# Performance work log

Hardware: AMD Instinct MI355X
Metric: run time of the kernel (lower is better)

Reference implementation:

```python
import jax, jax.numpy as jnp
import numpy as np

B, T, D = 1, 2048, 1024
H = 16
HD = D // H
K = 4
FF = 4 * D
LAYERS = 24
EPS = 1.1920929e-07  # torch.finfo(float32).eps, RMSNorm default


def setup_inputs() -> dict:
    key = jax.random.key(0)
    ks = jax.random.split(key, 16)
    s = 0.02
    return {
        "x": jax.random.normal(ks[0], (B, T, D), jnp.float32),
        "gamma": jax.random.uniform(ks[1], (D,), jnp.float32),
        "beta": jax.random.normal(ks[2], (D,), jnp.float32) * 0.1,
        "iter_scale": jax.random.uniform(ks[3], (1,), jnp.float32),
        "qkv_bases": jax.random.normal(ks[4], (K, 3 * D, D), jnp.float32) * s,
        "o_bases": jax.random.normal(ks[5], (K, D, D), jnp.float32) * s,
        "gate_bases": jax.random.normal(ks[6], (K, FF, D), jnp.float32) * s,
        "up_bases": jax.random.normal(ks[7], (K, FF, D), jnp.float32) * s,
        "down_bases": jax.random.normal(ks[8], (K, D, FF), jnp.float32) * s,
        "alpha_qkv": jax.random.normal(ks[9], (LAYERS, K), jnp.float32) * 0.1 + jnp.eye(LAYERS, K)[:, :K] * 0.0 + jnp.concatenate([jnp.ones((LAYERS, 1)), jnp.zeros((LAYERS, K - 1))], axis=1),
        "alpha_o": jnp.concatenate([jnp.ones((LAYERS, 1)), jnp.zeros((LAYERS, K - 1))], axis=1) + jax.random.normal(ks[10], (LAYERS, K)) * 0.1,
        "alpha_gate": jnp.concatenate([jnp.ones((LAYERS, 1)), jnp.zeros((LAYERS, K - 1))], axis=1) + jax.random.normal(ks[11], (LAYERS, K)) * 0.1,
        "alpha_up": jnp.concatenate([jnp.ones((LAYERS, 1)), jnp.zeros((LAYERS, K - 1))], axis=1) + jax.random.normal(ks[12], (LAYERS, K)) * 0.1,
        "alpha_down": jnp.concatenate([jnp.ones((LAYERS, 1)), jnp.zeros((LAYERS, K - 1))], axis=1) + jax.random.normal(ks[13], (LAYERS, K)) * 0.1,
        "norm1_w": jnp.ones((D,), jnp.float32),
        "norm2_w": jnp.ones((D,), jnp.float32),
        "layer_idx": 5,
    }


def _rmsnorm(x, w):
    return x * jax.lax.rsqrt(jnp.mean(x * x, axis=-1, keepdims=True) + EPS) * w


def reference(x, gamma, beta, iter_scale, qkv_bases, o_bases, gate_bases, up_bases,
              down_bases, alpha_qkv, alpha_o, alpha_gate, alpha_up, alpha_down,
              norm1_w, norm2_w, layer_idx):
    Bx, Tx, Dx = x.shape
    # --- attention sub-block ---
    h = _rmsnorm(x, norm1_w) * gamma + beta
    W_qkv = jnp.einsum('k,kij->ij', alpha_qkv[layer_idx], qkv_bases)  # [3D, D]
    qkv = jnp.einsum('btd,od->bto', h, W_qkv).reshape(Bx, Tx, 3, H, HD)
    qkv = jnp.transpose(qkv, (2, 0, 3, 1, 4))  # [3, B, H, T, HD]
    q, k, v = qkv[0], qkv[1], qkv[2]
    scores = jnp.einsum('bhqd,bhkd->bhqk', q, k) / jnp.sqrt(jnp.asarray(HD, x.dtype))
    causal = jnp.tril(jnp.ones((Tx, Tx), bool))
    scores = jnp.where(causal, scores, jnp.asarray(-jnp.inf, scores.dtype))
    attn = jax.nn.softmax(scores, axis=-1)
    out = jnp.einsum('bhqk,bhkd->bhqd', attn, v)
    out = jnp.transpose(out, (0, 2, 1, 3)).reshape(Bx, Tx, Dx)
    W_o = jnp.einsum('k,kij->ij', alpha_o[layer_idx], o_bases)
    x_attn = x + jnp.einsum('btd,od->bto', out, W_o)
    # --- SwiGLU FFN sub-block ---
    h2 = _rmsnorm(x_attn, norm2_w) * gamma + beta
    W_g = jnp.einsum('k,kij->ij', alpha_gate[layer_idx], gate_bases)
    W_u = jnp.einsum('k,kij->ij', alpha_up[layer_idx], up_bases)
    W_d = jnp.einsum('k,kij->ij', alpha_down[layer_idx], down_bases)
    gate = jnp.einsum('btd,fd->btf', h2, W_g)
    up = jnp.einsum('btd,fd->btf', h2, W_u)
    ffn_out = jnp.einsum('btf,df->btd', jax.nn.silu(gate) * up, W_d)
    block_out = x_attn + ffn_out
    return x + (block_out - x) * iter_scale
```

## Files before the change

### kernel.cpp

```cpp
#include <hip/hip_runtime.h>
#include <hip/hip_bf16.h>
#include <math.h>

typedef __bf16 bf16;
typedef __bf16 bf16x8 __attribute__((ext_vector_type(8)));
typedef __bf16 bf16x4 __attribute__((ext_vector_type(4)));
typedef float f32x4 __attribute__((ext_vector_type(4)));

#define EPSc 1.1920929e-07f
#define LOG2E 1.44269504f

static __device__ __forceinline__ void glds16(const void* g, void* l) {
  __builtin_amdgcn_global_load_lds((const __attribute__((address_space(1))) void*)g,
                                   (__attribute__((address_space(3))) void*)l, 16, 0, 0);
}

static __device__ __forceinline__ bf16x4 comb4(const float* b0, const float* b1,
                                               const float* b2, const float* b3,
                                               float a0, float a1, float a2, float a3) {
  float4 v0 = *(const float4*)b0, v1 = *(const float4*)b1;
  float4 v2 = *(const float4*)b2, v3 = *(const float4*)b3;
  bf16x4 o;
  o[0] = (bf16)(a0*v0.x + a1*v1.x + a2*v2.x + a3*v3.x);
  o[1] = (bf16)(a0*v0.y + a1*v1.y + a2*v2.y + a3*v3.y);
  o[2] = (bf16)(a0*v0.z + a1*v1.z + a2*v2.z + a3*v3.z);
  o[3] = (bf16)(a0*v0.w + a1*v1.w + a2*v2.w + a3*v3.w);
  return o;
}

__global__ __launch_bounds__(256)
void prep1(const float* __restrict__ qkv_b, const float* __restrict__ a_qkv,
           const float* __restrict__ o_b,   const float* __restrict__ a_o,
           const float* __restrict__ x, const float* __restrict__ n1w,
           const float* __restrict__ gamma, const float* __restrict__ beta,
           const int* __restrict__ lidx,
           bf16* __restrict__ Wqkv, bf16* __restrict__ Wo, bf16* __restrict__ hbuf) {
  const int bid = blockIdx.x, tid = threadIdx.x;
  if (bid < 4096) {
    int li = lidx[0];
    const float* base; const float* al; bf16* out; size_t flat, n;
    if (bid < 3072) { base = qkv_b; al = a_qkv; out = Wqkv; flat = (size_t)bid << 10; n = (size_t)3072*1024; }
    else            { base = o_b;   al = a_o;   out = Wo;   flat = (size_t)(bid-3072) << 10; n = (size_t)1024*1024; }
    float a0 = al[li*4], a1 = al[li*4+1], a2 = al[li*4+2], a3 = al[li*4+3];
    size_t off = flat + tid*4;
    bf16x4 o = comb4(base+off, base+n+off, base+2*n+off, base+3*n+off, a0, a1, a2, a3);
    *(bf16x4*)&out[off] = o;
  } else {
    int row = bid - 4096, t = tid;
    const float4* xr = (const float4*)(x + (size_t)row*1024);
    float4 v = xr[t];
    float ss = v.x*v.x + v.y*v.y + v.z*v.z + v.w*v.w;
    #pragma unroll
    for (int off = 32; off > 0; off >>= 1) ss += __shfl_down(ss, off, 64);
    __shared__ float red[4];
    if ((t & 63) == 0) red[t >> 6] = ss;
    __syncthreads();
    float tot = red[0] + red[1] + red[2] + red[3];
    float r = rsqrtf(tot * (1.0f/1024.0f) + EPSc);
    float4 wv = ((const float4*)n1w)[t];
    float4 gv = ((const float4*)gamma)[t];
    float4 bv = ((const float4*)beta)[t];
    bf16x4 o;
    o[0] = (bf16)(v.x*r*wv.x*gv.x + bv.x);
    o[1] = (bf16)(v.y*r*wv.y*gv.y + bv.y);
    o[2] = (bf16)(v.z*r*wv.z*gv.z + bv.z);
    o[3] = (bf16)(v.w*r*wv.w*gv.w + bv.w);
    *(bf16x4*)&hbuf[(size_t)row*1024 + t*4] = o;
  }
}

__global__ __launch_bounds__(256) void rmsnorm_k(const float* __restrict__ x,
                                                 const float* __restrict__ w,
                                                 const float* __restrict__ gamma,
                                                 const float* __restrict__ beta,
                                                 bf16* __restrict__ out) {
  int row = blockIdx.x, t = threadIdx.x;
  const float4* xr = (const float4*)(x + (size_t)row*1024);
  float4 v = xr[t];
  float ss = v.x*v.x + v.y*v.y + v.z*v.z + v.w*v.w;
  #pragma unroll
  for (int off = 32; off > 0; off >>= 1) ss += __shfl_down(ss, off, 64);
  __shared__ float red[4];
  if ((t & 63) == 0) red[t >> 6] = ss;
  __syncthreads();
  float tot = red[0] + red[1] + red[2] + red[3];
  float r = rsqrtf(tot * (1.0f/1024.0f) + EPSc);
  float4 wv = ((const float4*)w)[t];
  float4 gv = ((const float4*)gamma)[t];
  float4 bv = ((const float4*)beta)[t];
  bf16x4 o;
  o[0] = (bf16)(v.x*r*wv.x*gv.x + bv.x);
  o[1] = (bf16)(v.y*r*wv.y*gv.y + bv.y);
  o[2] = (bf16)(v.z*r*wv.z*gv.z + bv.z);
  o[3] = (bf16)(v.w*r*wv.w*gv.w + bv.w);
  *(bf16x4*)&out[(size_t)row*1024 + t*4] = o;
}

template<int EP, int NTW>
__global__ __launch_bounds__(256)
void gemm_bt(const bf16* __restrict__ A, const bf16* __restrict__ Bw,
             int M, int N, int K, int gx,
             float* __restrict__ outf, bf16* __restrict__ outb,
             const float* __restrict__ auxf, const float* __restrict__ auxf2,
             const float* __restrict__ iscale) {
  constexpr int BN = NTW * 32;
  __shared__ __align__(16) bf16 As[2][128*64];
  __shared__ __align__(16) bf16 Bs[2][BN*64];
  const int nwg = gridDim.x;
  const int orig = blockIdx.x;
  const int wg = (orig & 7) * (nwg >> 3) + (orig >> 3);
  const int tn0 = (wg % gx) * BN, tm0 = (wg / gx) * 128;
  const int tid = threadIdx.x, wave = tid >> 6, lane = tid & 63;
  const int lr = lane & 15, lg = lane >> 4;
  const int wr = wave >> 1, wc = wave & 1;
  f32x4 acc[4][NTW] = {};
  const int rs = lane >> 3, cs = (lane & 7) * 8;

  const bf16* Abase = A + (size_t)tm0 * K;
  const bf16* Bbase = Bw + (size_t)tn0 * K;

  auto stage = [&](bf16* as, bf16* bs, int k0) {
    #pragma unroll
    for (int j = 0; j < 4; ++j) {
      int chunk = wave*4 + j;
      int r = chunk*8 + rs;
      glds16(Abase + (size_t)r*K + k0 + cs, as + chunk*512 + lane*8);
    }
    #pragma unroll
    for (int j = 0; j < NTW; ++j) {
      int chunk = wave*NTW + j;
      int r = chunk*8 + rs;
      glds16(Bbase + (size_t)r*K + k0 + cs, bs + chunk*512 + lane*8);
    }
  };
  auto comp = [&](const bf16* as, const bf16* bs) {
    #pragma unroll
    for (int kk = 0; kk < 2; ++kk) {
      bf16x8 av[4], bv[NTW];
      #pragma unroll
      for (int m = 0; m < 4; ++m) av[m] = *(const bf16x8*)&as[(wr*64 + m*16 + lr)*64 + kk*32 + lg*8];
      #pragma unroll
      for (int n = 0; n < NTW; ++n) bv[n] = *(const bf16x8*)&bs[(wc*NTW*16 + n*16 + lr)*64 + kk*32 + lg*8];
      #pragma unroll
      for (int m = 0; m < 4; ++m)
        #pragma unroll
        for (int n = 0; n < NTW; ++n)
          acc[m][n] = __builtin_amdgcn_mfma_f32_16x16x32_bf16(av[m], bv[n], acc[m][n], 0, 0, 0);
    }
  };

  bf16 *a0 = As[0], *a1 = As[1], *b0 = Bs[0], *b1 = Bs[1];
  stage(a0, b0, 0);
  __syncthreads();
  for (int k0 = 64; k0 < K; k0 += 64) {
    stage(a1, b1, k0);
    comp(a0, b0);
    __syncthreads();
    bf16* t;
    t = a0; a0 = a1; a1 = t;
    t = b0; b0 = b1; b1 = t;
  }
  comp(a0, b0);

  float its = 0.f;
  if constexpr (EP == 4) its = iscale[0];

  if constexpr (EP == 5) {
    #pragma unroll
    for (int m = 0; m < 4; ++m)
      #pragma unroll
      for (int j = 0; j < NTW/2; ++j)
        #pragma unroll
        for (int i = 0; i < 4; ++i) {
          int row = tm0 + wr*64 + m*16 + lg*4 + i;
          int col = (tn0 >> 1) + wc*(NTW*8) + j*16 + lr;
          float g = acc[m][2*j][i], u = acc[m][2*j+1][i];
          float s = g / (1.f + __builtin_amdgcn_exp2f(-g * LOG2E));
          outb[(size_t)row * (N >> 1) + col] = (bf16)(s * u);
        }
  } else {
    #pragma unroll
    for (int m = 0; m < 4; ++m)
      #pragma unroll
      for (int n = 0; n < NTW; ++n)
        #pragma unroll
        for (int i = 0; i < 4; ++i) {
          int row = tm0 + wr*64 + m*16 + lg*4 + i;
          int col = tn0 + wc*NTW*16 + n*16 + lr;
          size_t idx = (size_t)row * N + col;
          float v = acc[m][n][i];
          if constexpr (EP == 0) outb[idx] = (bf16)v;
          else if constexpr (EP == 1) outf[idx] = auxf[idx] + v;
          else if constexpr (EP == 4) {
            float xv = auxf[idx], xa = auxf2[idx];
            outf[idx] = xv + (xa + v - xv) * its;
          }
        }
  }
}

__global__ __launch_bounds__(256)
void attn_mega(const bf16* __restrict__ qkv, bf16* __restrict__ out,
               const float* __restrict__ gate_b, const float* __restrict__ up_b,
               const float* __restrict__ down_b,
               const float* __restrict__ a_gate, const float* __restrict__ a_up,
               const float* __restrict__ a_down, const int* __restrict__ lidx,
               bf16* __restrict__ Wgu, bf16* __restrict__ Wd) {
  __shared__ __align__(16) bf16 Ks[2][64*72];
  __shared__ __align__(16) bf16 Vt[2][64*66];
  __shared__ __align__(16) bf16 Ps[4][16*68];
  const int bid = blockIdx.x;
  const int tid = threadIdx.x;

  if (bid >= 512) {
    const int cb = bid - 512;
    int li = lidx[0];
    float g0 = a_gate[li*4], g1 = a_gate[li*4+1], g2 = a_gate[li*4+2], g3 = a_gate[li*4+3];
    float u0 = a_up[li*4],   u1 = a_up[li*4+1],   u2 = a_up[li*4+2],   u3 = a_up[li*4+3];
    float d0 = a_down[li*4], d1 = a_down[li*4+1], d2 = a_down[li*4+2], d3 = a_down[li*4+3];
    const size_t PS = (size_t)4096 * 1024;
    for (int it = 0; it < 24; ++it) {
      int chunk = cb * 24 + it;
      if (chunk < 8192) {
        int r = chunk, w = r & 31;
        int f = ((r >> 5) << 4) + (w & 15);
        const float* base = (w < 16) ? gate_b : up_b;
        float a0 = (w < 16) ? g0 : u0, a1 = (w < 16) ? g1 : u1;
        float a2 = (w < 16) ? g2 : u2, a3 = (w < 16) ? g3 : u3;
        size_t src = (size_t)f*1024 + tid*4;
        bf16x4 o = comb4(base+src, base+PS+src, base+2*PS+src, base+3*PS+src, a0, a1, a2, a3);
        *(bf16x4*)&Wgu[((size_t)r << 10) + tid*4] = o;
      } else {
        size_t off = ((size_t)(chunk - 8192) << 10) + tid*4;
        bf16x4 o = comb4(down_b+off, down_b+PS+off, down_b+2*PS+off, down_b+3*PS+off, d0, d1, d2, d3);
        *(bf16x4*)&Wd[off] = o;
      }
    }
    return;
  }

  const int qb = 31 - (bid >> 4);
  const int h = (bid & 7) + 8 * ((bid >> 3) & 1);
  const int wave = tid >> 6, lane = tid & 63;
  const int lr = lane & 15, lg = lane >> 4;
  const int q0 = qb * 64;

  bf16x8 qf[2];
  {
    const bf16* qrow = qkv + (size_t)(q0 + wave*16 + lr)*3072 + h*64;
    qf[0] = *(const bf16x8*)(qrow + lg*8);
    qf[1] = *(const bf16x8*)(qrow + 32 + lg*8);
  }
  f32x4 o[4] = {};
  float mrow[4], lrow[4];
  #pragma unroll
  for (int i = 0; i < 4; ++i) { mrow[i] = -__builtin_inff(); lrow[i] = 0.f; }

  const int r0 = tid >> 3, r1 = (tid + 256) >> 3;
  const int c0 = (tid & 7) << 3;
  const bf16* kb = qkv + 1024 + h*64 + c0;
  const bf16* vb = qkv + 2048 + h*64 + c0;

  bf16x8 kreg[2], vreg[2];
  auto stage_load = [&](int kv0) {
    kreg[0] = *(const bf16x8*)(kb + (size_t)(kv0 + r0)*3072);
    kreg[1] = *(const bf16x8*)(kb + (size_t)(kv0 + r1)*3072);
    vreg[0] = *(const bf16x8*)(vb + (size_t)(kv0 + r0)*3072);
    vreg[1] = *(const bf16x8*)(vb + (size_t)(kv0 + r1)*3072);
  };
  auto stage_write = [&](int buf) {
    *(bf16x8*)&Ks[buf][r0*72 + c0] = kreg[0];
    *(bf16x8*)&Ks[buf][r1*72 + c0] = kreg[1];
    #pragma unroll
    for (int e = 0; e < 8; ++e) Vt[buf][(c0 + e)*66 + r0] = vreg[0][e];
    #pragma unroll
    for (int e = 0; e < 8; ++e) Vt[buf][(c0 + e)*66 + r1] = vreg[1][e];
  };

  stage_load(0);
  stage_write(0);
  __syncthreads();
  int cur = 0;

  const float C = 0.125f * LOG2E;

  for (int t = 0; t <= qb; ++t) {
    const int kv0 = t * 64;
    if (t < qb) stage_load(kv0 + 64);

    f32x4 s[4] = {};
    __builtin_amdgcn_s_setprio(1);
    #pragma unroll
    for (int n = 0; n < 4; ++n) {
      bf16x8 k0f = *(const bf16x8*)&Ks[cur][(n*16 + lr)*72 + lg*8];
      s[n] = __builtin_amdgcn_mfma_f32_16x16x32_bf16(qf[0], k0f, s[n], 0, 0, 0);
      bf16x8 k1f = *(const bf16x8*)&Ks[cur][(n*16 + lr)*72 + 32 + lg*8];
      s[n] = __builtin_amdgcn_mfma_f32_16x16x32_bf16(qf[1], k1f, s[n], 0, 0, 0);
    }
    __builtin_amdgcn_s_setprio(0);
    const int qbase = q0 + wave*16 + lg*4;
    #pragma unroll
    for (int n = 0; n < 4; ++n)
      #pragma unroll
      for (int i = 0; i < 4; ++i) {
        float sv = s[n][i] * C;
        s[n][i] = (kv0 + n*16 + lr <= qbase + i) ? sv : -__builtin_inff();
      }
    float mnew[4], fac[4], rsum[4];
    #pragma unroll
    for (int i = 0; i < 4; ++i) mnew[i] = fmaxf(fmaxf(s[0][i], s[1][i]), fmaxf(s[2][i], s[3][i]));
    #pragma unroll
    for (int i = 0; i < 4; ++i)
      #pragma unroll
      for (int off = 1; off < 16; off <<= 1) mnew[i] = fmaxf(mnew[i], __shfl_xor(mnew[i], off, 64));
    #pragma unroll
    for (int i = 0; i < 4; ++i) {
      float mt = fmaxf(mrow[i], mnew[i]);
      fac[i] = __builtin_amdgcn_exp2f(mrow[i] - mt);
      mrow[i] = mt;
    }
    #pragma unroll
    for (int n = 0; n < 4; ++n)
      #pragma unroll
      for (int i = 0; i < 4; ++i) s[n][i] = __builtin_amdgcn_exp2f(s[n][i] - mrow[i]);
    #pragma unroll
    for (int i = 0; i < 4; ++i) rsum[i] = s[0][i] + s[1][i] + s[2][i] + s[3][i];
    #pragma unroll
    for (int i = 0; i < 4; ++i)
      #pragma unroll
      for (int off = 1; off < 16; off <<= 1) rsum[i] += __shfl_xor(rsum[i], off, 64);
    #pragma unroll
    for (int i = 0; i < 4; ++i) lrow[i] = lrow[i]*fac[i] + rsum[i];
    #pragma unroll
    for (int nd = 0; nd < 4; ++nd)
      #pragma unroll
      for (int i = 0; i < 4; ++i) o[nd][i] *= fac[i];
    #pragma unroll
    for (int n = 0; n < 4; ++n)
      #pragma unroll
      for (int i = 0; i < 4; ++i) Ps[wave][(lg*4 + i)*68 + n*16 + lr] = (bf16)s[n][i];
    asm volatile("s_waitcnt lgkmcnt(0)" ::: "memory");
    __builtin_amdgcn_s_setprio(1);
    #pragma unroll
    for (int kk = 0; kk < 2; ++kk) {
      bf16x8 pf = *(const bf16x8*)&Ps[wave][lr*68 + kk*32 + lg*8];
      #pragma unroll
      for (int nd = 0; nd < 4; ++nd) {
        bf16x8 vf = *(const bf16x8*)&Vt[cur][(nd*16 + lr)*66 + kk*32 + lg*8];
        o[nd] = __builtin_amdgcn_mfma_f32_16x16x32_bf16(pf, vf, o[nd], 0, 0, 0);
      }
    }
    __builtin_amdgcn_s_setprio(0);
    if (t < qb) {
      stage_write(cur ^ 1);
      __syncthreads();
      cur ^= 1;
    }
  }
  #pragma unroll
  for (int i = 0; i < 4; ++i) {
    float inv = 1.f / lrow[i];
    #pragma unroll
    for (int nd = 0; nd < 4; ++nd)
      out[(size_t)(q0 + wave*16 + lg*4 + i)*1024 + h*64 + nd*16 + lr] = (bf16)(o[nd][i]*inv);
  }
}

extern "C" void kernel_launch(void* const* d_in, const int* in_sizes, int n_in,
                              void* d_out, int out_size, void* d_ws, size_t ws_size,
                              hipStream_t stream) {
  const float* x        = (const float*)d_in[0];
  const float* gamma    = (const float*)d_in[1];
  const float* beta     = (const float*)d_in[2];
  const float* iscale   = (const float*)d_in[3];
  const float* qkv_b    = (const float*)d_in[4];
  const float* o_b      = (const float*)d_in[5];
  const float* gate_b   = (const float*)d_in[6];
  const float* up_b     = (const float*)d_in[7];
  const float* down_b   = (const float*)d_in[8];
  const float* a_qkv    = (const float*)d_in[9];
  const float* a_o      = (const float*)d_in[10];
  const float* a_gate   = (const float*)d_in[11];
  const float* a_up     = (const float*)d_in[12];
  const float* a_down   = (const float*)d_in[13];
  const float* n1w      = (const float*)d_in[14];
  const float* n2w      = (const float*)d_in[15];
  const int*   lidx     = (const int*)d_in[16];

  char* p = (char*)d_ws;
  auto alloc = [&](size_t bytes) { char* r = p; p += (bytes + 255) & ~(size_t)255; return r; };
  bf16*  Wqkv = (bf16*)alloc((size_t)3072*1024*2);
  bf16*  Wo   = (bf16*)alloc((size_t)1024*1024*2);
  bf16*  Wgu  = (bf16*)alloc((size_t)8192*1024*2);
  bf16*  Wd   = (bf16*)alloc((size_t)1024*4096*2);
  bf16*  hbuf = (bf16*)alloc((size_t)2048*1024*2);
  bf16*  qkvb = (bf16*)alloc((size_t)2048*3072*2);
  bf16*  attn = (bf16*)alloc((size_t)2048*1024*2);
  float* xat  = (float*)alloc((size_t)2048*1024*4);
  bf16*  h2   = (bf16*)alloc((size_t)2048*1024*2);
  bf16*  act  = (bf16*)alloc((size_t)2048*4096*2);
  float* out  = (float*)d_out;

  prep1<<<6144, 256, 0, stream>>>(qkv_b, a_qkv, o_b, a_o, x, n1w, gamma, beta, lidx,
                                  Wqkv, Wo, hbuf);
  gemm_bt<0,4><<<24*16, 256, 0, stream>>>(hbuf, Wqkv, 2048, 3072, 1024, 24,
                                          nullptr, qkvb, nullptr, nullptr, nullptr);
  attn_mega<<<1024, 256, 0, stream>>>(qkvb, attn, gate_b, up_b, down_b,
                                      a_gate, a_up, a_down, lidx, Wgu, Wd);
  gemm_bt<1,2><<<16*16, 256, 0, stream>>>(attn, Wo, 2048, 1024, 1024, 16,
                                          xat, nullptr, x, nullptr, nullptr);
  rmsnorm_k<<<2048, 256, 0, stream>>>(xat, n2w, gamma, beta, h2);
  gemm_bt<5,4><<<64*16, 256, 0, stream>>>(h2, Wgu, 2048, 8192, 1024, 64,
                                          nullptr, act, nullptr, nullptr, nullptr);
  gemm_bt<4,2><<<16*16, 256, 0, stream>>>(act, Wd, 2048, 1024, 4096, 16,
                                          out, nullptr, x, xat, iscale);
}
```

Measured before the change: 225.3 us.

## Split down-projection along K, lazy softmax rescale, reorder weight-combine blocks

Breaks the down-projection GEMM (K=4096) into two K=2048 GEMMs that write fp32 partials into reused workspace, then combines them with the residual and iter_scale in a separate reduce kernel. Attention gets a lazy online-softmax rescale that only updates the running max when it grows past a threshold, applies the causal mask only on the diagonal tile, and folds the scale into an fma. The weight-combine blocks move to the front of the attention launch with a strided chunk mapping and fewer blocks. The two launches run back to back on one stream, so the K-split does not add concurrency and mainly adds an extra fp32 write and read of the partials.

```diff
diff --git a/kernel.cpp b/kernel.cpp
--- a/kernel.cpp
+++ b/kernel.cpp
@@ -99,7 +99,7 @@
 template<int EP, int NTW>
 __global__ __launch_bounds__(256)
 void gemm_bt(const bf16* __restrict__ A, const bf16* __restrict__ Bw,
-             int M, int N, int K, int gx,
+             int M, int N, int K, int lda, int ldb, int gx,
              float* __restrict__ outf, bf16* __restrict__ outb,
              const float* __restrict__ auxf, const float* __restrict__ auxf2,
              const float* __restrict__ iscale) {
@@ -116,21 +116,21 @@
   f32x4 acc[4][NTW] = {};
   const int rs = lane >> 3, cs = (lane & 7) * 8;
 
-  const bf16* Abase = A + (size_t)tm0 * K;
-  const bf16* Bbase = Bw + (size_t)tn0 * K;
+  const bf16* Abase = A + (size_t)tm0 * lda;
+  const bf16* Bbase = Bw + (size_t)tn0 * ldb;
 
   auto stage = [&](bf16* as, bf16* bs, int k0) {
     #pragma unroll
     for (int j = 0; j < 4; ++j) {
       int chunk = wave*4 + j;
       int r = chunk*8 + rs;
-      glds16(Abase + (size_t)r*K + k0 + cs, as + chunk*512 + lane*8);
+      glds16(Abase + (size_t)r*lda + k0 + cs, as + chunk*512 + lane*8);
     }
     #pragma unroll
     for (int j = 0; j < NTW; ++j) {
       int chunk = wave*NTW + j;
       int r = chunk*8 + rs;
-      glds16(Bbase + (size_t)r*K + k0 + cs, bs + chunk*512 + lane*8);
+      glds16(Bbase + (size_t)r*ldb + k0 + cs, bs + chunk*512 + lane*8);
     }
   };
   auto comp = [&](const bf16* as, const bf16* bs) {
@@ -194,9 +194,25 @@
           else if constexpr (EP == 4) {
             float xv = auxf[idx], xa = auxf2[idx];
             outf[idx] = xv + (xa + v - xv) * its;
-          }
+          } else if constexpr (EP == 6) outf[idx] = v;
         }
   }
+}
+
+__global__ __launch_bounds__(256)
+void reduce2(const float* __restrict__ p0, const float* __restrict__ p1,
+             const float* __restrict__ x, const float* __restrict__ xat,
+             const float* __restrict__ iscale, float* __restrict__ out) {
+  size_t i = (size_t)blockIdx.x * 256 + threadIdx.x;
+  float its = iscale[0];
+  float4 a = ((const float4*)p0)[i], b = ((const float4*)p1)[i];
+  float4 xv = ((const float4*)x)[i], xa = ((const float4*)xat)[i];
+  float4 o;
+  o.x = xv.x + (xa.x + a.x + b.x - xv.x) * its;
+  o.y = xv.y + (xa.y + a.y + b.y - xv.y) * its;
+  o.z = xv.z + (xa.z + a.z + b.z - xv.z) * its;
+  o.w = xv.w + (xa.w + a.w + b.w - xv.w) * its;
+  ((float4*)out)[i] = o;
 }
 
 __global__ __launch_bounds__(256)
@@ -212,15 +228,15 @@
   const int bid = blockIdx.x;
   const int tid = threadIdx.x;
 
-  if (bid >= 512) {
-    const int cb = bid - 512;
+  if (bid < 256) {
+    const int cb = bid;
     int li = lidx[0];
     float g0 = a_gate[li*4], g1 = a_gate[li*4+1], g2 = a_gate[li*4+2], g3 = a_gate[li*4+3];
     float u0 = a_up[li*4],   u1 = a_up[li*4+1],   u2 = a_up[li*4+2],   u3 = a_up[li*4+3];
     float d0 = a_down[li*4], d1 = a_down[li*4+1], d2 = a_down[li*4+2], d3 = a_down[li*4+3];
     const size_t PS = (size_t)4096 * 1024;
-    for (int it = 0; it < 24; ++it) {
-      int chunk = cb * 24 + it;
+    for (int it = 0; it < 48; ++it) {
+      int chunk = it * 256 + cb;
       if (chunk < 8192) {
         int r = chunk, w = r & 31;
         int f = ((r >> 5) << 4) + (w & 15);
@@ -239,8 +255,9 @@
     return;
   }
 
-  const int qb = 31 - (bid >> 4);
-  const int h = (bid & 7) + 8 * ((bid >> 3) & 1);
+  const int a = bid - 256;
+  const int qb = 31 - (a >> 4);
+  const int h = (a & 7) + 8 * ((a >> 3) & 1);
   const int wave = tid >> 6, lane = tid & 63;
   const int lr = lane & 15, lg = lane >> 4;
   const int q0 = qb * 64;
@@ -298,43 +315,52 @@
       s[n] = __builtin_amdgcn_mfma_f32_16x16x32_bf16(qf[1], k1f, s[n], 0, 0, 0);
     }
     __builtin_amdgcn_s_setprio(0);
-    const int qbase = q0 + wave*16 + lg*4;
+
+    if (t == qb) {
+      const int qbase = q0 + wave*16 + lg*4;
+      #pragma unroll
+      for (int n = 0; n < 4; ++n)
+        #pragma unroll
+        for (int i = 0; i < 4; ++i)
+          if (kv0 + n*16 + lr > qbase + i) s[n][i] = -__builtin_inff();
+    }
+
+    float mnewr[4], pmn[4];
+    #pragma unroll
+    for (int i = 0; i < 4; ++i) mnewr[i] = fmaxf(fmaxf(s[0][i], s[1][i]), fmaxf(s[2][i], s[3][i]));
+    #pragma unroll
+    for (int i = 0; i < 4; ++i)
+      #pragma unroll
+      for (int off = 1; off < 16; off <<= 1) mnewr[i] = fmaxf(mnewr[i], __shfl_xor(mnewr[i], off, 64));
+    bool grow = false;
+    #pragma unroll
+    for (int i = 0; i < 4; ++i) { pmn[i] = mnewr[i] * C; grow = grow || (pmn[i] > mrow[i] + 8.f); }
+    if (__any(grow)) {
+      #pragma unroll
+      for (int i = 0; i < 4; ++i) {
+        float mt = fmaxf(mrow[i], pmn[i]);
+        float fc = __builtin_amdgcn_exp2f(mrow[i] - mt);
+        mrow[i] = mt;
+        lrow[i] *= fc;
+        #pragma unroll
+        for (int nd = 0; nd < 4; ++nd) o[nd][i] *= fc;
+      }
+    }
+    float rsum[4] = {0.f, 0.f, 0.f, 0.f};
     #pragma unroll
     for (int n = 0; n < 4; ++n)
       #pragma unroll
       for (int i = 0; i < 4; ++i) {
-        float sv = s[n][i] * C;
-        s[n][i] = (kv0 + n*16 + lr <= qbase + i) ? sv : -__builtin_inff();
+        float e = __builtin_amdgcn_exp2f(__builtin_fmaf(s[n][i], C, -mrow[i]));
+        s[n][i] = e;
+        rsum[i] += e;
       }
-    float mnew[4], fac[4], rsum[4];
-    #pragma unroll
-    for (int i = 0; i < 4; ++i) mnew[i] = fmaxf(fmaxf(s[0][i], s[1][i]), fmaxf(s[2][i], s[3][i]));
     #pragma unroll
     for (int i = 0; i < 4; ++i)
       #pragma unroll
-      for (int off = 1; off < 16; off <<= 1) mnew[i] = fmaxf(mnew[i], __shfl_xor(mnew[i], off, 64));
-    #pragma unroll
-    for (int i = 0; i < 4; ++i) {
-      float mt = fmaxf(mrow[i], mnew[i]);
-      fac[i] = __builtin_amdgcn_exp2f(mrow[i] - mt);
-      mrow[i] = mt;
-    }
-    #pragma unroll
-    for (int n = 0; n < 4; ++n)
-      #pragma unroll
-      for (int i = 0; i < 4; ++i) s[n][i] = __builtin_amdgcn_exp2f(s[n][i] - mrow[i]);
-    #pragma unroll
-    for (int i = 0; i < 4; ++i) rsum[i] = s[0][i] + s[1][i] + s[2][i] + s[3][i];
-    #pragma unroll
-    for (int i = 0; i < 4; ++i)
-      #pragma unroll
       for (int off = 1; off < 16; off <<= 1) rsum[i] += __shfl_xor(rsum[i], off, 64);
     #pragma unroll
-    for (int i = 0; i < 4; ++i) lrow[i] = lrow[i]*fac[i] + rsum[i];
-    #pragma unroll
-    for (int nd = 0; nd < 4; ++nd)
-      #pragma unroll
-      for (int i = 0; i < 4; ++i) o[nd][i] *= fac[i];
+    for (int i = 0; i < 4; ++i) lrow[i] += rsum[i];
     #pragma unroll
     for (int n = 0; n < 4; ++n)
       #pragma unroll
@@ -400,18 +426,23 @@
   bf16*  h2   = (bf16*)alloc((size_t)2048*1024*2);
   bf16*  act  = (bf16*)alloc((size_t)2048*4096*2);
   float* out  = (float*)d_out;
+  float* part0 = (float*)Wqkv;
+  float* part1 = (float*)qkvb;
 
   prep1<<<6144, 256, 0, stream>>>(qkv_b, a_qkv, o_b, a_o, x, n1w, gamma, beta, lidx,
                                   Wqkv, Wo, hbuf);
-  gemm_bt<0,4><<<24*16, 256, 0, stream>>>(hbuf, Wqkv, 2048, 3072, 1024, 24,
+  gemm_bt<0,4><<<24*16, 256, 0, stream>>>(hbuf, Wqkv, 2048, 3072, 1024, 1024, 1024, 24,
                                           nullptr, qkvb, nullptr, nullptr, nullptr);
-  attn_mega<<<1024, 256, 0, stream>>>(qkvb, attn, gate_b, up_b, down_b,
-                                      a_gate, a_up, a_down, lidx, Wgu, Wd);
-  gemm_bt<1,2><<<16*16, 256, 0, stream>>>(attn, Wo, 2048, 1024, 1024, 16,
+  attn_mega<<<768, 256, 0, stream>>>(qkvb, attn, gate_b, up_b, down_b,
+                                     a_gate, a_up, a_down, lidx, Wgu, Wd);
+  gemm_bt<1,2><<<16*16, 256, 0, stream>>>(attn, Wo, 2048, 1024, 1024, 1024, 1024, 16,
                                           xat, nullptr, x, nullptr, nullptr);
   rmsnorm_k<<<2048, 256, 0, stream>>>(xat, n2w, gamma, beta, h2);
-  gemm_bt<5,4><<<64*16, 256, 0, stream>>>(h2, Wgu, 2048, 8192, 1024, 64,
+  gemm_bt<5,4><<<64*16, 256, 0, stream>>>(h2, Wgu, 2048, 8192, 1024, 1024, 1024, 64,
                                           nullptr, act, nullptr, nullptr, nullptr);
-  gemm_bt<4,2><<<16*16, 256, 0, stream>>>(act, Wd, 2048, 1024, 4096, 16,
-                                          out, nullptr, x, xat, iscale);
-}
+  gemm_bt<6,2><<<16*16, 256, 0, stream>>>(act, Wd, 2048, 1024, 2048, 4096, 4096, 16,
+                                          part0, nullptr, nullptr, nullptr, nullptr);
+  gemm_bt<6,2><<<16*16, 256, 0, stream>>>(act + 2048, Wd + 2048, 2048, 1024, 2048, 4096, 4096, 16,
+                                          part1, nullptr, nullptr, nullptr, nullptr);
+  reduce2<<<2048, 256, 0, stream>>>(part0, part1, x, xat, iscale, out);
+}
```

Result: slower. 234.9 us (+4.3%).
